# Performance work log

Hardware: AMD Instinct MI355X
Metric: run time of the kernel (lower is better)

## Reference

```python
import jax, jax.numpy as jnp
import numpy as np

WEIGHT = 1000.0      # start/end cell penalty
LONELY_W = 15.0      # cell lit outside cluster
CLUSTER_W = 5.0      # cell unlit inside cluster
CELL_W = 20.0        # cell on a shortest manhattan path
CSIZE_W = 12.0       # cluster-size penalty
GAP_W = 300.0        # gap-to-endpoint penalty
H = W = 10


def _md(y1, x1, y2, x2):
    return jnp.abs(y1 - y2) + jnp.abs(x1 - x2)


def _per_sample(result, points):
    # result: [H, W] float, points: [2, 2] int (row, col) of start and end
    p0y, p0x = points[0, 0], points[0, 1]
    p1y, p1x = points[1, 0], points[1, 1]
    base = _md(p0y, p0x, p1y, p1x)

    loss_start = (2.0 - (result[p0y, p0x] + result[p1y, p1x])) * WEIGHT

    # 8-connected flood fill from start over cells whose value rounds to 1.
    mask = jnp.round(result) == 1.0
    seed = jnp.zeros((H, W), bool).at[p0y, p0x].set(True)

    def dilate(_, c):
        p = jnp.pad(c, 1)
        nb = (p[:-2, :-2] | p[:-2, 1:-1] | p[:-2, 2:] |
              p[1:-1, :-2] | p[1:-1, 2:] |
              p[2:, :-2] | p[2:, 1:-1] | p[2:, 2:])
        return c | (nb & mask)

    # 8-connected diameter of a 10x10 grid is 9; H+W iterations is a safe bound.
    cluster = jax.lax.fori_loop(0, H + W, dilate, seed)

    rows = jnp.arange(H)[:, None]
    cols = jnp.arange(W)[None, :]

    # per-cell manhattan detour penalty
    d2 = _md(rows, cols, p0y, p0x) + _md(rows, cols, p1y, p1x)
    delta = (d2 - base).astype(result.dtype)
    single_cell = jnp.sum(jnp.where(delta == 0.0,
                                    (1.0 - result) * CELL_W,
                                    result * delta * 0.5))

    # NB: the original tests [column, row] membership against [row, col]
    # cluster entries -> transposed membership map. Faithfully reproduced.
    in_cl = cluster.T
    csize = jnp.sum(cluster).astype(result.dtype)
    lonelyness = jnp.sum(jnp.where(in_cl, (1.0 - result) * CLUSTER_W,
                                   result * LONELY_W))
    cluster_size_pen = jnp.sum(jnp.where(in_cl, result * csize * CSIZE_W, 0.0))

    # nearest cluster cell to the end point (strict improvement over base)
    dist_end = _md(rows, cols, p1y, p1x)
    masked = jnp.where(cluster, dist_end, H * W + 10).reshape(-1)
    idx = jnp.argmin(masked)
    minval = masked[idx]
    better = minval < base
    ny = jnp.where(better, idx // W, p0y)
    nx = jnp.where(better, idx % W, p0x)
    gap = jnp.minimum(base, minval)

    oy = p1y - ny
    ox = p1x - nx

    def upd(cond, cy, cx, st):
        by, bx, bg = st
        d = _md(cy, cx, p1y, p1x)
        b = cond & (d < bg)
        return (jnp.where(b, cy, by), jnp.where(b, cx, bx), jnp.where(b, d, bg))

    st = (ny, nx, gap)
    c = ox < 0
    st = upd(c, ny, nx - 1, st)
    st = upd(c & (ny != 0), ny - 1, nx - 1, st)
    st = upd(c & (ny != H - 1), ny + 1, nx - 1, st)
    c = ox > 0
    st = upd(c, ny, nx + 1, st)
    st = upd(c & (ny != 0), ny - 1, nx + 1, st)
    st = upd(c & (ny != H - 1), ny + 1, nx + 1, st)
    st = upd(oy < 0, ny - 1, nx, st)
    st = upd(oy > 0, ny + 1, nx, st)
    ncy = jnp.clip(st[0], 0, H - 1)
    ncx = jnp.clip(st[1], 0, W - 1)

    gap_pen = gap.astype(result.dtype) * GAP_W * (1.0 - result[ncy, ncx])

    return loss_start + lonelyness + single_cell + cluster_size_pen + gap_pen


def setup_inputs() -> dict:
    key = jax.random.key(0)
    k1, k2 = jax.random.split(key)
    B = 262144
    result_given = jax.random.uniform(k1, (B, 1, H, W), dtype=jnp.float32)
    points_given = jax.random.randint(k2, (B, 2, 2), 0, 10, dtype=jnp.int64 if jax.config.jax_enable_x64 else jnp.int32)
    return {"result_given": result_given, "points_given": points_given}


def reference(result_given, points_given):
    losses = jax.vmap(_per_sample)(result_given[:, 0], points_given)
    return jnp.sum(losses).reshape(1)
```

## Files before the change

kernel.cpp:

```cpp
#include <hip/hip_runtime.h>
#include <cstdint>

#define GH 10
#define GW 10

__global__ __launch_bounds__(256, 4) void custom_loss_kernel(
    const float* __restrict__ result,
    const int* __restrict__ points,
    float* __restrict__ out,
    int B)
{
    const int tid = blockIdx.x * blockDim.x + threadIdx.x;
    const int s = tid >> 2;
    const int q = tid & 3;
    float loss = 0.f;
    if (s < B) {
        const float* __restrict__ r = result + (size_t)s * 100;
        const int4 p = ((const int4*)points)[s];
        const int p0y = p.x, p0x = p.y, p1y = p.z, p1x = p.w;
        const int dy0 = abs(p0y - p1y), dx0 = abs(p0x - p1x);
        const int base0 = dy0 + dx0;
        const int idx0 = p0y * GW + p0x;
        const int idx1 = p1y * GW + p1x;
        const float rs = r[idx0];
        const float re = r[idx1];

        float4 v4[7];
#pragma unroll
        for (int i = 0; i < 6; ++i) v4[i] = ((const float4*)r)[4 * i + q];
        v4[6] = make_float4(0.f, 0.f, 0.f, 0.f);
        if (q == 0) v4[6] = ((const float4*)r)[24];

        const uint64_t M50 = (1ull << 50) - 1;
        float sum_p = 0.f, sc_p = 0.f, box_p = 0.f;
        uint64_t mlo = 0, mhi = 0;
#pragma unroll
        for (int i = 0; i < 7; ++i) {
            const int kbase = (i < 6) ? 4 * (4 * i + q) : (96 + 4 * q);
            const float vv[4] = {v4[i].x, v4[i].y, v4[i].z, v4[i].w};
            uint32_t nib = 0;
#pragma unroll
            for (int j = 0; j < 4; ++j) {
                const int flat = kbase + j;
                const int y = (flat * 205) >> 11;
                const int x = flat - 10 * y;
                const float v = vv[j];
                sum_p += v;
                const int af = abs(y - p0y) + abs(y - p1y) - dy0
                             + abs(x - p0x) + abs(x - p1x) - dx0;
                sc_p = fmaf((float)af, v, sc_p);
                box_p += (af == 0) ? v : 0.f;
                nib |= (v > 0.5f) ? (1u << j) : 0u;
            }
            const uint64_t n64 = (uint64_t)nib;
            const int shhi = (kbase >= 50) ? (kbase - 50) : 0;
            mlo |= (kbase <= 44) ? (n64 << kbase)
                                 : ((kbase == 48) ? ((n64 & 3ull) << 48) : 0);
            mhi |= (kbase >= 52) ? (n64 << shhi)
                                 : ((kbase == 48) ? (n64 >> 2) : 0);
        }
        sum_p += __shfl_xor(sum_p, 1); sum_p += __shfl_xor(sum_p, 2);
        sc_p  += __shfl_xor(sc_p, 1);  sc_p  += __shfl_xor(sc_p, 2);
        box_p += __shfl_xor(box_p, 1); box_p += __shfl_xor(box_p, 2);
        mlo |= (uint64_t)__shfl_xor((unsigned long long)mlo, 1);
        mlo |= (uint64_t)__shfl_xor((unsigned long long)mlo, 2);
        mhi |= (uint64_t)__shfl_xor((unsigned long long)mhi, 1);
        mhi |= (uint64_t)__shfl_xor((unsigned long long)mhi, 2);
        const float sum_all = sum_p, sc = sc_p, boxSum = box_p;

        const uint64_t C0  = 0x10040100401ull;
        const uint64_t NC0 = M50 & ~C0;
        const uint64_t NC9 = M50 & ~(C0 << 9);
        uint64_t clo = 0, chi = 0;
        if (idx0 < 50) clo = 1ull << idx0; else chi = 1ull << (idx0 - 50);
#pragma unroll 1
        for (int it = 0; it < GH + GW; ++it) {
            const uint64_t hlo = clo | ((clo << 1) & NC0) | ((clo >> 1) & NC9);
            const uint64_t hhi = chi | ((chi << 1) & NC0) | ((chi >> 1) & NC9);
            uint64_t nlo = (hlo | (hlo << 10) | (hlo >> 10) | ((hhi & 0x3FFull) << 40)) & mlo;
            uint64_t nhi = (hhi | (hhi << 10) | (hhi >> 10) | (hlo >> 40)) & mhi;
            nlo |= clo; nhi |= chi;
            if (nlo == clo && nhi == chi) break;
            clo = nlo; chi = nhi;
        }
        const int K = __popcll(clo) + __popcll(chi);

        float st_p = 0.f;
#pragma unroll
        for (int i = 0; i < 7; ++i) {
            const int kbase = (i < 6) ? 4 * (4 * i + q) : (96 + 4 * q);
            const float vv[4] = {v4[i].x, v4[i].y, v4[i].z, v4[i].w};
#pragma unroll
            for (int j = 0; j < 4; ++j) {
                const int flat = kbase + j;
                const int y = (flat * 205) >> 11;
                const int x = flat - 10 * y;
                const int tr = x * 10 + y;
                const int trs = (tr >= 50) ? (tr - 50) : tr;
                const uint64_t w = (tr >= 50) ? chi : clo;
                st_p = fmaf((float)((w >> trs) & 1ull), vv[j], st_p);
            }
        }
        st_p += __shfl_xor(st_p, 1); st_p += __shfl_xor(st_p, 2);
        const float S_T = st_p;

        int bestd = 1000, bidx = 0;
#pragma unroll
        for (int y = 0; y < GH; ++y) {
            const uint32_t rb = (uint32_t)((y < 5 ? (clo >> (10 * y))
                                                  : (chi >> (10 * (y - 5)))) & 0x3FFull);
            const uint32_t left  = rb & ((2u << p1x) - 1);
            const uint32_t right = rb >> p1x;
            const int dl = left  ? (p1x - (31 - __builtin_clz(left))) : 1000;
            const int dr = right ? __builtin_ctz(right) : 1000;
            int dx, xx;
            if (dl <= dr) { dx = dl; xx = p1x - dl; }
            else          { dx = dr; xx = p1x + dr; }
            const int d = abs(y - p1y) + dx;
            if (rb && d < bestd) { bestd = d; bidx = y * GW + xx; }
        }

        const bool better = bestd < base0;
        const int ny = better ? bidx / 10 : p0y;
        const int nx = better ? bidx % 10 : p0x;
        const int gap = min(base0, bestd);

        int by = ny, bx = nx, bg = gap;
        const int oy = p1y - ny, ox = p1x - nx;
        auto upd = [&](bool cond, int cy, int cx) {
            const int d = abs(cy - p1y) + abs(cx - p1x);
            if (cond && (d < bg)) { by = cy; bx = cx; bg = d; }
        };
        upd(ox < 0,                     ny,     nx - 1);
        upd((ox < 0) && (ny != 0),      ny - 1, nx - 1);
        upd((ox < 0) && (ny != GH - 1), ny + 1, nx - 1);
        upd(ox > 0,                     ny,     nx + 1);
        upd((ox > 0) && (ny != 0),      ny - 1, nx + 1);
        upd((ox > 0) && (ny != GH - 1), ny + 1, nx + 1);
        upd(oy < 0,                     ny - 1, nx);
        upd(oy > 0,                     ny + 1, nx);
        const int ncy = min(max(by, 0), GH - 1);
        const int ncx = min(max(bx, 0), GW - 1);
        const float rn = r[ncy * GW + ncx];

        const float csf = (float)K;
        const float nboxf = (float)((dy0 + 1) * (dx0 + 1));
        const float loss_start = (2.f - (rs + re)) * 1000.f;
        const float lon = 5.f * csf + 15.f * sum_all - 20.f * S_T;
        const float single_cell = 0.5f * sc + 20.f * (nboxf - boxSum);
        const float cpen = 12.f * csf * S_T;
        const float gap_pen = (float)gap * 300.f * (1.f - rn);
        loss = loss_start + lon + single_cell + cpen + gap_pen;
        if (q != 0) loss = 0.f;
    }

#pragma unroll
    for (int off = 32; off > 0; off >>= 1)
        loss += __shfl_down(loss, off);
    __shared__ float wsum[4];
    const int lane = threadIdx.x & 63;
    const int wid = threadIdx.x >> 6;
    if (lane == 0) wsum[wid] = loss;
    __syncthreads();
    if (threadIdx.x == 0)
        atomicAdd(out, wsum[0] + wsum[1] + wsum[2] + wsum[3]);
}

extern "C" void kernel_launch(void* const* d_in, const int* in_sizes, int n_in,
                              void* d_out, int out_size, void* d_ws, size_t ws_size,
                              hipStream_t stream)
{
    const float* result = (const float*)d_in[0];
    const int* points   = (const int*)d_in[1];
    float* out = (float*)d_out;
    const int B = in_sizes[0] / 100;
    hipMemsetAsync(out, 0, sizeof(float), stream);
    const int block = 256;
    const int grid = (4 * B + block - 1) / block;
    custom_loss_kernel<<<grid, block, 0, stream>>>(result, points, out, B);
}
```

Measured before the change: 181.9 us.

## Split flood fill and nearest-cell search across quad lanes, simplify detour math

The 8-connected flood fill now runs with each pair of lanes in a quad owning one 50-bit half of the grid, exchanging boundary rows by shuffle each iteration. The nearest-cluster-cell search is split by row across the four lanes and combined with a packed-key min reduction. The detour cost is separated into row and column float sums with base subtracted once, and the transposed-membership sum uses bit extraction per float4 group. The aim is to cut per-thread ALU work on 64-bit masks. In exchange it adds shuffles inside the loop and relies on the argmin tie-break matching through key ordering.

```diff
diff --git a/kernel.cpp b/kernel.cpp
--- a/kernel.cpp
+++ b/kernel.cpp
@@ -24,6 +24,10 @@
         const int idx1 = p1y * GW + p1x;
         const float rs = r[idx0];
         const float re = r[idx1];
+        const float p0yf = (float)p0y, p0xf = (float)p0x;
+        const float p1yf = (float)p1y, p1xf = (float)p1x;
+        const float dy0f = (float)dy0, dx0f = (float)dx0;
+        const float basef = (float)base0;
 
         float4 v4[7];
 #pragma unroll
@@ -31,25 +35,30 @@
         v4[6] = make_float4(0.f, 0.f, 0.f, 0.f);
         if (q == 0) v4[6] = ((const float4*)r)[24];
 
-        const uint64_t M50 = (1ull << 50) - 1;
-        float sum_p = 0.f, sc_p = 0.f, box_p = 0.f;
+        float sum_p = 0.f, scA = 0.f, scB = 0.f, box_p = 0.f;
         uint64_t mlo = 0, mhi = 0;
 #pragma unroll
         for (int i = 0; i < 7; ++i) {
             const int kbase = (i < 6) ? 4 * (4 * i + q) : (96 + 4 * q);
+            const int y0 = (kbase * 205) >> 11;
+            const int x0 = kbase - 10 * y0;
+            const float y0f = (float)y0, x0f = (float)x0;
+            const float sy0 = fabsf(y0f - p0yf) + fabsf(y0f - p1yf);
+            const float sy1 = fabsf(y0f + 1.f - p0yf) + fabsf(y0f + 1.f - p1yf);
+            const bool wrap = (x0 == 8);
             const float vv[4] = {v4[i].x, v4[i].y, v4[i].z, v4[i].w};
             uint32_t nib = 0;
 #pragma unroll
             for (int j = 0; j < 4; ++j) {
-                const int flat = kbase + j;
-                const int y = (flat * 205) >> 11;
-                const int x = flat - 10 * y;
+                const bool w = wrap && (j >= 2);
+                const float xf = x0f + (w ? (float)(j - 10) : (float)j);
+                const float syj = w ? sy1 : sy0;
                 const float v = vv[j];
+                const float sx = fabsf(xf - p0xf) + fabsf(xf - p1xf);
                 sum_p += v;
-                const int af = abs(y - p0y) + abs(y - p1y) - dy0
-                             + abs(x - p0x) + abs(x - p1x) - dx0;
-                sc_p = fmaf((float)af, v, sc_p);
-                box_p += (af == 0) ? v : 0.f;
+                scA = fmaf(syj, v, scA);
+                scB = fmaf(sx, v, scB);
+                box_p += ((sx == dx0f) & (syj == dy0f)) ? v : 0.f;
                 nib |= (v > 0.5f) ? (1u << j) : 0u;
             }
             const uint64_t n64 = (uint64_t)nib;
@@ -60,65 +69,90 @@
                                  : ((kbase == 48) ? (n64 >> 2) : 0);
         }
         sum_p += __shfl_xor(sum_p, 1); sum_p += __shfl_xor(sum_p, 2);
-        sc_p  += __shfl_xor(sc_p, 1);  sc_p  += __shfl_xor(sc_p, 2);
+        scA   += __shfl_xor(scA, 1);   scA   += __shfl_xor(scA, 2);
+        scB   += __shfl_xor(scB, 1);   scB   += __shfl_xor(scB, 2);
         box_p += __shfl_xor(box_p, 1); box_p += __shfl_xor(box_p, 2);
         mlo |= (uint64_t)__shfl_xor((unsigned long long)mlo, 1);
         mlo |= (uint64_t)__shfl_xor((unsigned long long)mlo, 2);
         mhi |= (uint64_t)__shfl_xor((unsigned long long)mhi, 1);
         mhi |= (uint64_t)__shfl_xor((unsigned long long)mhi, 2);
-        const float sum_all = sum_p, sc = sc_p, boxSum = box_p;
-
+        const float sum_all = sum_p, boxSum = box_p;
+        const float sc = fmaf(-basef, sum_all, scA + scB);
+
+        const uint64_t M50 = (1ull << 50) - 1;
         const uint64_t C0  = 0x10040100401ull;
         const uint64_t NC0 = M50 & ~C0;
         const uint64_t NC9 = M50 & ~(C0 << 9);
-        uint64_t clo = 0, chi = 0;
-        if (idx0 < 50) clo = 1ull << idx0; else chi = 1ull << (idx0 - 50);
+        const int half = q >> 1;
+        const uint64_t mw = half ? mhi : mlo;
+        uint64_t c = 0;
+        if (half == 0 && idx0 < 50)  c = 1ull << idx0;
+        if (half == 1 && idx0 >= 50) c = 1ull << (idx0 - 50);
 #pragma unroll 1
         for (int it = 0; it < GH + GW; ++it) {
-            const uint64_t hlo = clo | ((clo << 1) & NC0) | ((clo >> 1) & NC9);
-            const uint64_t hhi = chi | ((chi << 1) & NC0) | ((chi >> 1) & NC9);
-            uint64_t nlo = (hlo | (hlo << 10) | (hlo >> 10) | ((hhi & 0x3FFull) << 40)) & mlo;
-            uint64_t nhi = (hhi | (hhi << 10) | (hhi >> 10) | (hlo >> 40)) & mhi;
-            nlo |= clo; nhi |= chi;
-            if (nlo == clo && nhi == chi) break;
-            clo = nlo; chi = nhi;
-        }
-        const int K = __popcll(clo) + __popcll(chi);
+            const uint64_t ho = c | ((c << 1) & NC0) | ((c >> 1) & NC9);
+            const uint64_t hoth = (uint64_t)__shfl_xor((unsigned long long)ho, 2);
+            const uint64_t inc = half ? (hoth >> 40) : ((hoth & 0x3FFull) << 40);
+            const uint64_t n = ((ho | (ho << 10) | (ho >> 10) | inc) & mw) | c;
+            int ch = (n != c) ? 1 : 0;
+            ch += __shfl_xor(ch, 2);
+            c = n;
+            if (!ch) break;
+        }
+        int Kh = __popcll(c);
+        const int K = Kh + __shfl_xor(Kh, 2);
+        const uint64_t coth = (uint64_t)__shfl_xor((unsigned long long)c, 2);
+        const uint64_t clo = half ? coth : c;
+        const uint64_t chi = half ? c : coth;
+        const uint32_t cl32 = (uint32_t)clo;
 
         float st_p = 0.f;
 #pragma unroll
         for (int i = 0; i < 7; ++i) {
             const int kbase = (i < 6) ? 4 * (4 * i + q) : (96 + 4 * q);
+            const int y0 = (kbase * 205) >> 11;
+            const int x0 = kbase - 10 * y0;
+            const int s0 = x0 * 10 + y0;
+            const uint64_t tA = (clo >> (s0 & 63)) | (chi << ((50 - s0) & 63));
+            const uint64_t tB = chi >> ((s0 - 50) & 63);
+            const uint32_t tl = (uint32_t)((s0 < 50) ? tA : tB);
+            uint32_t nib = (tl & 1u) | ((tl >> 9) & 2u) |
+                           ((tl >> 18) & 4u) | ((tl >> 27) & 8u);
+            if (x0 == 8) {
+                const uint32_t b2 = (cl32 >> (y0 + 1)) & 1u;
+                const uint32_t b3 = (cl32 >> (y0 + 11)) & 1u;
+                nib = (nib & 3u) | (b2 << 2) | (b3 << 3);
+            }
             const float vv[4] = {v4[i].x, v4[i].y, v4[i].z, v4[i].w};
 #pragma unroll
-            for (int j = 0; j < 4; ++j) {
-                const int flat = kbase + j;
-                const int y = (flat * 205) >> 11;
-                const int x = flat - 10 * y;
-                const int tr = x * 10 + y;
-                const int trs = (tr >= 50) ? (tr - 50) : tr;
-                const uint64_t w = (tr >= 50) ? chi : clo;
-                st_p = fmaf((float)((w >> trs) & 1ull), vv[j], st_p);
-            }
+            for (int j = 0; j < 4; ++j)
+                st_p += (nib & (1u << j)) ? vv[j] : 0.f;
         }
         st_p += __shfl_xor(st_p, 1); st_p += __shfl_xor(st_p, 2);
         const float S_T = st_p;
 
-        int bestd = 1000, bidx = 0;
-#pragma unroll
-        for (int y = 0; y < GH; ++y) {
-            const uint32_t rb = (uint32_t)((y < 5 ? (clo >> (10 * y))
-                                                  : (chi >> (10 * (y - 5)))) & 0x3FFull);
-            const uint32_t left  = rb & ((2u << p1x) - 1);
-            const uint32_t right = rb >> p1x;
-            const int dl = left  ? (p1x - (31 - __builtin_clz(left))) : 1000;
-            const int dr = right ? __builtin_ctz(right) : 1000;
-            int dx, xx;
-            if (dl <= dr) { dx = dl; xx = p1x - dl; }
-            else          { dx = dr; xx = p1x + dr; }
-            const int d = abs(y - p1y) + dx;
-            if (rb && d < bestd) { bestd = d; bidx = y * GW + xx; }
-        }
+        int bestkey = 0x7FFFFFFF;
+#pragma unroll
+        for (int k = 0; k < 3; ++k) {
+            const int y = q + 4 * k;
+            if (y < GH) {
+                const uint32_t rb = (uint32_t)(((y < 5) ? (clo >> (10 * y))
+                                                        : (chi >> (10 * (y - 5)))) & 0x3FFull);
+                const uint32_t left  = rb & ((2u << p1x) - 1);
+                const uint32_t right = rb >> p1x;
+                const int dl = left  ? (p1x - (31 - __builtin_clz(left))) : 1000;
+                const int dr = right ? __builtin_ctz(right) : 1000;
+                int dx, xx;
+                if (dl <= dr) { dx = dl; xx = p1x - dl; }
+                else          { dx = dr; xx = p1x + dr; }
+                const int key = ((abs(y - p1y) + dx) << 7) | (y * GW + xx);
+                if (rb && key < bestkey) bestkey = key;
+            }
+        }
+        bestkey = min(bestkey, __shfl_xor(bestkey, 1));
+        bestkey = min(bestkey, __shfl_xor(bestkey, 2));
+        const int bestd = bestkey >> 7;
+        const int bidx = bestkey & 127;
 
         const bool better = bestd < base0;
         const int ny = better ? bidx / 10 : p0y;
```

After: 185.3 us. Within noise of the previous version (+1.9%).
